# Kernel optimization log

Measured on AMD Instinct MI355X. Metric: run time of the kernel, lower is better.

The kernel has to match this reference:

```python
import jax, jax.numpy as jnp
import numpy as np

# dims: T=max seq len, B=batch, D=d_embed, H=d_hidden, NR=n_roles, NH=n_heads
T, B, D, H = 512, 64, 512, 1024
NR, NH = 64, 8
HD = H // NH  # per-head hidden


def _lengths():
    # monotonically non-increasing lengths -> valid PackedSequence batch_sizes
    return np.round(np.linspace(T, T // 4, B)).astype(np.int32)


def _packed_idx(lengths):
    batch_sizes = np.array([(lengths > t).sum() for t in range(T)], dtype=np.int64)
    # flat row index into padded [T*B] for each packed token (time-major)
    return np.concatenate([t * B + np.arange(batch_sizes[t]) for t in range(T)]).astype(np.int32)


def setup_inputs() -> dict:
    key = jax.random.key(0)
    ks = jax.random.split(key, 12)
    lengths = _lengths()
    idx = _packed_idx(lengths)
    total = int(idx.shape[0])  # 20480
    s = lambda k, shape, sc=1.0: (jax.random.normal(k, shape, jnp.float32) * sc)
    return {
        'x': s(ks[0], (total, D)),
        'idx': jnp.asarray(idx),
        'lengths': jnp.asarray(lengths),
        'basis0': s(ks[1], (NR, H)),  # frozen role basis (requires_grad=False)
        'basis1': s(ks[2], (NR, H)),
        'Wx0': s(ks[3], (2 * H, D), 0.02), 'bx0': jnp.zeros((2 * H,), jnp.float32),
        'Wh0': s(ks[4], (2 * H, H), 0.02), 'bh0': jnp.zeros((2 * H,), jnp.float32),
        'Wv0': s(ks[5], (2 * H, H), 0.02), 'bv0': jnp.zeros((2 * H,), jnp.float32),
        'Wx1': s(ks[6], (2 * H, H), 0.02), 'bx1': jnp.zeros((2 * H,), jnp.float32),
        'Wh1': s(ks[7], (2 * H, H), 0.02), 'bh1': jnp.zeros((2 * H,), jnp.float32),
        'Wv1': s(ks[8], (2 * H, H), 0.02), 'bv1': jnp.zeros((2 * H,), jnp.float32),
    }


def _tpru_layer(x2fg_pad, Wh, bh, r, u, lengths):
    """Run the sequential TPRU recurrence over padded [T,B,2H] precomputed x2fg.

    Replaces the packed per-timestep Python loop (output[p:q] slicing with
    varying batch sizes) with a full-batch lax.scan; rows of padded timesteps
    beyond a sequence's length are computed but never read into output or hn,
    so the math on valid positions is identical.
    """
    h0 = jnp.zeros((B, H), x2fg_pad.dtype)
    hn0 = jnp.zeros((B, H), x2fg_pad.dtype)

    def step(carry, inp):
        h, hn = carry
        x2fg_t, t = inp
        fg = h @ Wh.T + bh + x2fg_t                 # [B, 2H]
        f, g = jnp.split(fg, 2, axis=-1)
        fh = f.reshape(B, NH, HD)
        # unbind: attention over roles per head
        scores = jnp.einsum('bnd,rnd->brn', fh, r)   # [B, NR, NH]
        attn = jax.nn.softmax(scores, axis=1)
        # bind: weighted sum of unbinding vectors
        bind = jnp.einsum('brn,rnd->bnd', attn, u).reshape(B, H)
        gate = jax.nn.sigmoid(g)
        h_new = gate * jnp.tanh(bind) + (1.0 - gate) * h
        # hn captures hidden at each sequence's final valid step
        hn = jnp.where((lengths == t + 1)[:, None], h_new, hn)
        return (h_new, hn), h_new

    (_, hn), hs = jax.lax.scan(step, (h0, hn0), (x2fg_pad, jnp.arange(T)))
    return hs, hn  # hs: [T, B, H]


def reference(x, idx, lengths, basis0, basis1, Wx0, bx0, Wh0, bh0, Wv0, bv0,
              Wx1, bx1, Wh1, bh1, Wv1, bv1):
    # unpack packed data [total, D] into padded [T, B, D]
    x_pad = jnp.zeros((T * B, D), x.dtype).at[idx].set(x).reshape(T, B, D)
    # layer 0
    x2fg = x_pad @ Wx0.T + bx0                       # [T, B, 2H]
    v = (basis0 @ Wv0.T + bv0).reshape(NR, NH, 2 * HD)
    hs, hn0 = _tpru_layer(x2fg, Wh0, bh0, v[..., :HD], v[..., HD:], lengths)
    # layer 1 (input dim is now H)
    x2fg = hs @ Wx1.T + bx1
    v = (basis1 @ Wv1.T + bv1).reshape(NR, NH, 2 * HD)
    hs, hn1 = _tpru_layer(x2fg, Wh1, bh1, v[..., :HD], v[..., HD:], lengths)
    # repack output (time-major packed order, matching PackedSequence.data)
    packed = hs.reshape(T * B, H)[idx]               # [total, H]
    hn = jnp.stack([hn0, hn1])                       # [n_layers, B, H]
    return packed, hn
```

## Files before the change

kernel.cpp:

```cpp
#include <hip/hip_runtime.h>

typedef _Float16 f16;
typedef _Float16 f16x2 __attribute__((ext_vector_type(2)));
typedef _Float16 f16x4 __attribute__((ext_vector_type(4)));
typedef _Float16 f16x8 __attribute__((ext_vector_type(8)));
typedef float    f32x4 __attribute__((ext_vector_type(4)));

#define TT   512
#define BB   64
#define DD   512
#define HH   1024
#define H2   2048
#define NR_  64
#define NH_  8
#define HD_  128
#define MROWS (TT*BB)
#define RWG  64

#define ALOAD32(p)   __hip_atomic_load((p),  __ATOMIC_RELAXED, __HIP_MEMORY_SCOPE_AGENT)
#define ALOAD64(p)   __hip_atomic_load((p),  __ATOMIC_RELAXED, __HIP_MEMORY_SCOPE_AGENT)
#define ASTORE(p,v)  __hip_atomic_store((p), (v), __ATOMIC_RELAXED, __HIP_MEMORY_SCOPE_AGENT)

__global__ void k_cvt(const float* __restrict__ s, f16* __restrict__ d, int n) {
  int i = blockIdx.x * blockDim.x + threadIdx.x;
  int st = gridDim.x * blockDim.x;
  for (; i < n; i += st) d[i] = (f16)s[i];
}

__global__ void k_scatter(const float* __restrict__ x, const int* __restrict__ idx,
                          f16* __restrict__ xpad, int total) {
  int i = blockIdx.x * blockDim.x + threadIdx.x;
  int st = gridDim.x * blockDim.x;
  int n = total * DD;
  for (; i < n; i += st) {
    int p = i >> 9;
    int j = i & (DD - 1);
    xpad[(size_t)idx[p] * DD + j] = (f16)x[i];
  }
}

__global__ void k_inv(const int* __restrict__ idx, int* __restrict__ inv, int total) {
  int i = blockIdx.x * blockDim.x + threadIdx.x;
  if (i < total) inv[idx[i]] = i;
}

__global__ __launch_bounds__(256)
void k_gemm(const f16* __restrict__ A, const f16* __restrict__ Bw,
            const float* __restrict__ bias, f16* __restrict__ C,
            int N, int K, int Mvalid) {
  __shared__ __align__(16) f16 As[128 * 32];
  __shared__ __align__(16) f16 Bs[128 * 32];
  const int tid  = threadIdx.x;
  const int lane = tid & 63;
  const int wave = tid >> 6;
  const int m0 = blockIdx.y * 128;
  const int n0 = blockIdx.x * 128;
  const int mw = (wave >> 1) * 64;
  const int nw = (wave & 1) * 64;
  const int NT = K >> 5;
  const int c0 = tid * 2;

  float4 pa[2], pb[2];
  auto fetch = [&](int kt) {
#pragma unroll
    for (int i = 0; i < 2; ++i) {
      int c = c0 + i;
      int row = c >> 2, kc = c & 3;
      pa[i] = *(const float4*)&A [(size_t)(m0 + row) * K + kt * 32 + kc * 8];
      pb[i] = *(const float4*)&Bw[(size_t)(n0 + row) * K + kt * 32 + kc * 8];
    }
  };

  f32x4 acc[4][4] = {};
  fetch(0);
  for (int kt = 0; kt < NT; ++kt) {
    __syncthreads();
#pragma unroll
    for (int i = 0; i < 2; ++i) {
      int c = c0 + i;
      *(float4*)&As[c * 8] = pa[i];
      *(float4*)&Bs[c * 8] = pb[i];
    }
    __syncthreads();
    if (kt + 1 < NT) fetch(kt + 1);
    f16x8 af[4], bf[4];
#pragma unroll
    for (int i = 0; i < 4; ++i) {
      af[i] = *(const f16x8*)&As[(mw + i * 16 + (lane & 15)) * 32 + (lane >> 4) * 8];
      bf[i] = *(const f16x8*)&Bs[(nw + i * 16 + (lane & 15)) * 32 + (lane >> 4) * 8];
    }
#pragma unroll
    for (int i = 0; i < 4; ++i)
#pragma unroll
      for (int j = 0; j < 4; ++j)
        acc[i][j] = __builtin_amdgcn_mfma_f32_16x16x32_f16(af[i], bf[j], acc[i][j], 0, 0, 0);
  }

#pragma unroll
  for (int j = 0; j < 4; ++j) {
    int col = n0 + nw + j * 16 + (lane & 15);
    float bv = bias[col];
#pragma unroll
    for (int i = 0; i < 4; ++i) {
#pragma unroll
      for (int r = 0; r < 4; ++r) {
        int row = m0 + mw + i * 16 + (lane >> 4) * 4 + r;
        if (row < Mvalid) C[(size_t)row * N + col] = (f16)(acc[i][j][r] + bv);
      }
    }
  }
}

__device__ __forceinline__ void gbar(int* flags, int epoch) {
  __syncthreads();
  const int tid = threadIdx.x;
  if (tid == 0) ASTORE(&flags[blockIdx.x], epoch);
  if (tid < RWG) {
    while (ALOAD32(&flags[tid]) < epoch) __builtin_amdgcn_s_sleep(1);
  }
  __syncthreads();
}

__global__ __launch_bounds__(512, 2)
void k_rec(const f16* __restrict__ Wh16, const float* __restrict__ bh,
           const f16* __restrict__ v16,  const f16* __restrict__ x2fg,
           f16* __restrict__ hfrag, float* __restrict__ fgbuf,
           f16* __restrict__ hs_out, float* __restrict__ out_packed,
           float* __restrict__ hn_out,
           const int* __restrict__ inv, const int* __restrict__ lgt,
           int* __restrict__ flags, int epoch0)
{
  __shared__ __align__(16) f16   Wlds[32 * 2 * 64 * 8];
  __shared__ __align__(16) f16x4 Rq[32 * 64];
  __shared__ __align__(16) f16x4 Uq[16 * 2 * 64];
  __shared__ __align__(16) f32x4 pbuf[8][64];
  __shared__ __align__(16) float fbuf[8][128];
  __shared__ __align__(16) float abuf[8][64];

  const int tid  = threadIdx.x;
  const int lane = tid & 63;
  const int wave = tid >> 6;
  const int wg   = blockIdx.x;
  const int cs   = wg;
  const int rt   = wave & 3;
  const int kh   = wave >> 2;
  const int nh   = wg >> 3;
  const int b    = ((wg & 7) << 3) + wave;
  const int cf   = nh * HD_;

  for (int i = tid; i < 32 * 2 * 64; i += 512) {
    int kk = i >> 7;
    int nt = (i >> 6) & 1;
    int ln = i & 63;
    int col = cs * 32 + nt * 16 + (ln & 15);
    int kg  = kk * 32 + (ln >> 4) * 8;
    *(float4*)&Wlds[(size_t)i * 8] = *(const float4*)&Wh16[(size_t)col * HH + kg];
  }
  for (int e = tid; e < 32 * 64; e += 512) {
    int i = e >> 6, role = e & 63;
    Rq[e] = *(const f16x4*)&v16[(size_t)role * H2 + nh * 256 + 4 * i];
  }
  for (int e = tid; e < 16 * 2 * 64; e += 512) {
    int i = e >> 7, half = (e >> 6) & 1, l = e & 63;
    int r0 = 4 * i + 2 * half;
    const f16* u0 = &v16[(size_t)r0 * H2 + nh * 256 + 128 + 2 * l];
    const f16* u1 = &v16[(size_t)(r0 + 1) * H2 + nh * 256 + 128 + 2 * l];
    f16x4 tv; tv.x = u0[0]; tv.y = u0[1]; tv.z = u1[0]; tv.w = u1[1];
    Uq[e] = tv;
  }
  __syncthreads();

  const int d0 = cf + 2 * lane;
  const float2 bf2 = *(const float2*)&bh[d0];
  const float2 bg2 = *(const float2*)&bh[HH + d0];
  const int lb = lgt[b];
  float ho0 = 0.f, ho1 = 0.f;
  int ep = epoch0;
  const char* hb0 = (const char*)hfrag + (((size_t)kh * 64 + rt) * 64 + lane) * 16;
  const char* fp  = (const char*)fgbuf + (((size_t)b * H2) + d0) * 4;
  const char* gp  = fp + (size_t)HH * 4;

  for (int t = 0; t < TT; ++t) {
    const size_t row = (size_t)t * BB + b;
    const f16* xr = x2fg + row * H2;
    f16x2 xf = *(const f16x2*)&xr[d0];
    f16x2 xg = *(const f16x2*)&xr[HH + d0];
    int   p  = inv[row];

    f32x4 acc0 = {0.f, 0.f, 0.f, 0.f}, acc1 = acc0;
    {
      float4 hb[16];
#pragma unroll
      for (int j = 0; j < 16; ++j) {
        asm volatile("global_load_dwordx4 %0, %1, off sc0 sc1"
                     : "=v"(hb[j]) : "v"(hb0 + (size_t)j * 4096));
      }
      asm volatile("s_waitcnt vmcnt(0)" ::: "memory");
      __builtin_amdgcn_sched_barrier(0);
#pragma unroll
      for (int j = 0; j < 16; ++j) {
        int kk = kh * 16 + j;
        f16x8 af = __builtin_bit_cast(f16x8, hb[j]);
        f16x8 b0 = *(const f16x8*)&Wlds[((kk * 2 + 0) * 64 + lane) * 8];
        f16x8 b1 = *(const f16x8*)&Wlds[((kk * 2 + 1) * 64 + lane) * 8];
        acc0 = __builtin_amdgcn_mfma_f32_16x16x32_f16(af, b0, acc0, 0, 0, 0);
        acc1 = __builtin_amdgcn_mfma_f32_16x16x32_f16(af, b1, acc1, 0, 0, 0);
      }
    }
    pbuf[wave][lane] = (kh == 0) ? acc1 : acc0;
    __syncthreads();
    {
      f32x4 acc = ((kh == 0) ? acc0 : acc1) + pbuf[wave ^ 4][lane];
      const int col = cs * 32 + kh * 16 + (lane & 15);
      const int r0  = rt * 16 + (lane >> 4) * 4;
#pragma unroll
      for (int r = 0; r < 4; ++r) ASTORE(&fgbuf[(size_t)(r0 + r) * H2 + col], acc[r]);
    }
    gbar(flags, ++ep);

    float2 fv, gv;
    asm volatile("global_load_dwordx2 %0, %1, off sc0 sc1" : "=v"(fv) : "v"(fp));
    asm volatile("global_load_dwordx2 %0, %1, off sc0 sc1" : "=v"(gv) : "v"(gp));
    asm volatile("s_waitcnt vmcnt(0)" ::: "memory");
    __builtin_amdgcn_sched_barrier(0);
    float f0 = fv.x + bf2.x + (float)xf.x;
    float f1 = fv.y + bf2.y + (float)xf.y;
    float g0 = gv.x + bg2.x + (float)xg.x;
    float g1 = gv.y + bg2.y + (float)xg.y;
    *(float2*)&fbuf[wave][2 * lane] = make_float2(f0, f1);
    float s = 0.f;
#pragma unroll
    for (int i = 0; i < 32; ++i) {
      float4 fvv = *(const float4*)&fbuf[wave][4 * i];
      f16x4 rv = Rq[i * 64 + lane];
      s = fmaf(fvv.x, (float)rv.x, s);
      s = fmaf(fvv.y, (float)rv.y, s);
      s = fmaf(fvv.z, (float)rv.z, s);
      s = fmaf(fvv.w, (float)rv.w, s);
    }
    float mx = s;
#pragma unroll
    for (int off = 32; off > 0; off >>= 1) mx = fmaxf(mx, __shfl_xor(mx, off));
    float e = expf(s - mx);
    float sum = e;
#pragma unroll
    for (int off = 32; off > 0; off >>= 1) sum += __shfl_xor(sum, off);
    abuf[wave][lane] = e / sum;
    float bd0 = 0.f, bd1 = 0.f;
#pragma unroll
    for (int i = 0; i < 16; ++i) {
      float4 av = *(const float4*)&abuf[wave][4 * i];
      f16x4 u01 = Uq[(i * 2 + 0) * 64 + lane];
      f16x4 u23 = Uq[(i * 2 + 1) * 64 + lane];
      bd0 = fmaf(av.x, (float)u01.x, bd0); bd1 = fmaf(av.x, (float)u01.y, bd1);
      bd0 = fmaf(av.y, (float)u01.z, bd0); bd1 = fmaf(av.y, (float)u01.w, bd1);
      bd0 = fmaf(av.z, (float)u23.x, bd0); bd1 = fmaf(av.z, (float)u23.y, bd1);
      bd0 = fmaf(av.w, (float)u23.z, bd0); bd1 = fmaf(av.w, (float)u23.w, bd1);
    }
    float gt0 = 1.f / (1.f + expf(-g0));
    float gt1 = 1.f / (1.f + expf(-g1));
    float hv0 = gt0 * tanhf(bd0) + (1.f - gt0) * ho0;
    float hv1 = gt1 * tanhf(bd1) + (1.f - gt1) * ho1;
    ho0 = hv0; ho1 = hv1;
    {
      const int k0 = d0;
      unsigned hp = (unsigned)__builtin_bit_cast(unsigned short, (f16)hv0)
                  | ((unsigned)__builtin_bit_cast(unsigned short, (f16)hv1) << 16);
      size_t ui = (((size_t)(k0 >> 5) * 4 + (b >> 4)) * 64
                   + ((b & 15) + (((k0 >> 3) & 3) << 4))) * 4 + ((k0 & 7) >> 1);
      ASTORE((unsigned*)hfrag + ui, hp);
    }
    gbar(flags, ++ep);

    if (hs_out) {
      f16x2 hp2; hp2.x = (f16)ho0; hp2.y = (f16)ho1;
      *(f16x2*)&hs_out[row * HH + d0] = hp2;
    }
    if (out_packed && p >= 0) {
      *(float2*)&out_packed[(size_t)p * HH + d0] = make_float2(ho0, ho1);
    }
    if (lb == t + 1) {
      *(float2*)&hn_out[(size_t)b * HH + d0] = make_float2(ho0, ho1);
    }
  }
}

extern "C" void kernel_launch(void* const* d_in, const int* in_sizes, int n_in,
                              void* d_out, int out_size, void* d_ws, size_t ws_size,
                              hipStream_t stream) {
  const float* x      = (const float*)d_in[0];
  const int*   idx    = (const int*)d_in[1];
  const int*   lgt    = (const int*)d_in[2];
  const float* basis0 = (const float*)d_in[3];
  const float* basis1 = (const float*)d_in[4];
  const float* Wx0 = (const float*)d_in[5];  const float* bx0 = (const float*)d_in[6];
  const float* Wh0 = (const float*)d_in[7];  const float* bh0 = (const float*)d_in[8];
  const float* Wv0 = (const float*)d_in[9];  const float* bv0 = (const float*)d_in[10];
  const float* Wx1 = (const float*)d_in[11]; const float* bx1 = (const float*)d_in[12];
  const float* Wh1 = (const float*)d_in[13]; const float* bh1 = (const float*)d_in[14];
  const float* Wv1 = (const float*)d_in[15]; const float* bv1 = (const float*)d_in[16];
  const int total = in_sizes[1];

  char* ws = (char*)d_ws;
  size_t off = 0;
  auto alloc = [&](size_t bytes) -> void* {
    void* p = (void*)(ws + off);
    off += (bytes + 255) & ~(size_t)255;
    return p;
  };

  int*   flags   = (int*)alloc(RWG * 4);
  int*   inv     = (int*)alloc((size_t)MROWS * 4);
  f16*   xpad    = (f16*)alloc((size_t)MROWS * DD * 2);
  f16*   x2fg    = (f16*)alloc((size_t)MROWS * H2 * 2);
  f16*   hfrag   = (f16*)alloc((size_t)BB * HH * 2);
  float* fgbuf   = (float*)alloc((size_t)BB * H2 * 4);
  f16* Wx0h = (f16*)alloc((size_t)H2 * DD * 2);
  f16* Wh0h = (f16*)alloc((size_t)H2 * HH * 2);
  f16* Wv0h = (f16*)alloc((size_t)H2 * HH * 2);
  f16* Wx1h = (f16*)alloc((size_t)H2 * HH * 2);
  f16* Wh1h = (f16*)alloc((size_t)H2 * HH * 2);
  f16* Wv1h = (f16*)alloc((size_t)H2 * HH * 2);
  f16* bas0h = (f16*)alloc((size_t)128 * HH * 2);
  f16* bas1h = (f16*)alloc((size_t)128 * HH * 2);
  f16* v0h = (f16*)alloc((size_t)NR_ * H2 * 2);
  f16* v1h = (f16*)alloc((size_t)NR_ * H2 * 2);

  float* out = (float*)d_out;
  float* hn0 = out + (size_t)total * HH;
  float* hn1 = hn0 + (size_t)BB * HH;
  f16* hs0 = (f16*)d_out;

  (void)hipMemsetAsync(flags, 0, RWG * 4, stream);
  (void)hipMemsetAsync(inv, 0xFF, (size_t)MROWS * 4, stream);
  (void)hipMemsetAsync(xpad, 0, (size_t)MROWS * DD * 2, stream);
  (void)hipMemsetAsync(bas0h, 0, (size_t)128 * HH * 2, stream);
  (void)hipMemsetAsync(bas1h, 0, (size_t)128 * HH * 2, stream);
  (void)hipMemsetAsync(hfrag, 0, (size_t)BB * HH * 2, stream);

  k_cvt<<<512, 256, 0, stream>>>(Wx0, Wx0h, H2 * DD);
  k_cvt<<<512, 256, 0, stream>>>(Wh0, Wh0h, H2 * HH);
  k_cvt<<<512, 256, 0, stream>>>(Wv0, Wv0h, H2 * HH);
  k_cvt<<<512, 256, 0, stream>>>(Wx1, Wx1h, H2 * HH);
  k_cvt<<<512, 256, 0, stream>>>(Wh1, Wh1h, H2 * HH);
  k_cvt<<<512, 256, 0, stream>>>(Wv1, Wv1h, H2 * HH);
  k_cvt<<<64, 256, 0, stream>>>(basis0, bas0h, NR_ * HH);
  k_cvt<<<64, 256, 0, stream>>>(basis1, bas1h, NR_ * HH);
  k_scatter<<<2048, 256, 0, stream>>>(x, idx, xpad, total);
  k_inv<<<(total + 255) / 256, 256, 0, stream>>>(idx, inv, total);

  dim3 gv(16, 1);
  k_gemm<<<gv, 256, 0, stream>>>(bas0h, Wv0h, bv0, v0h, H2, HH, NR_);
  k_gemm<<<gv, 256, 0, stream>>>(bas1h, Wv1h, bv1, v1h, H2, HH, NR_);

  dim3 gx(H2 / 128, MROWS / 128);
  k_gemm<<<gx, 256, 0, stream>>>(xpad, Wx0h, bx0, x2fg, H2, DD, MROWS);

  k_rec<<<RWG, 512, 0, stream>>>(Wh0h, bh0, v0h, x2fg, hfrag, fgbuf,
                                 hs0, nullptr, hn0, inv, lgt, flags, 0);

  (void)hipMemsetAsync(hfrag, 0, (size_t)BB * HH * 2, stream);

  k_gemm<<<gx, 256, 0, stream>>>(hs0, Wx1h, bx1, x2fg, H2, HH, MROWS);

  k_rec<<<RWG, 512, 0, stream>>>(Wh1h, bh1, v1h, x2fg, hfrag, fgbuf,
                                 nullptr, out, hn1, inv, lgt, flags, 2 * TT);
}
```

Before: 11.52 ms.

## Split recurrent GEMM K across workgroup pairs with dual partial fg buffers

```diff
diff --git a/kernel.cpp b/kernel.cpp
--- a/kernel.cpp
+++ b/kernel.cpp
@@ -18,7 +18,6 @@
 #define RWG  64
 
 #define ALOAD32(p)   __hip_atomic_load((p),  __ATOMIC_RELAXED, __HIP_MEMORY_SCOPE_AGENT)
-#define ALOAD64(p)   __hip_atomic_load((p),  __ATOMIC_RELAXED, __HIP_MEMORY_SCOPE_AGENT)
 #define ASTORE(p,v)  __hip_atomic_store((p), (v), __ATOMIC_RELAXED, __HIP_MEMORY_SCOPE_AGENT)
 
 __global__ void k_cvt(const float* __restrict__ s, f16* __restrict__ d, int n) {
@@ -130,10 +129,10 @@
            const int* __restrict__ inv, const int* __restrict__ lgt,
            int* __restrict__ flags, int epoch0)
 {
-  __shared__ __align__(16) f16   Wlds[32 * 2 * 64 * 8];
+  __shared__ __align__(16) f16   Wlds[16 * 4 * 64 * 8];
   __shared__ __align__(16) f16x4 Rq[32 * 64];
   __shared__ __align__(16) f16x4 Uq[16 * 2 * 64];
-  __shared__ __align__(16) f32x4 pbuf[8][64];
+  __shared__ __align__(16) f32x4 pbuf[8][2][64];
   __shared__ __align__(16) float fbuf[8][128];
   __shared__ __align__(16) float abuf[8][64];
 
@@ -141,19 +140,20 @@
   const int lane = tid & 63;
   const int wave = tid >> 6;
   const int wg   = blockIdx.x;
-  const int cs   = wg;
+  const int cs   = wg >> 1;
+  const int kh   = wg & 1;
   const int rt   = wave & 3;
-  const int kh   = wave >> 2;
+  const int kq   = wave >> 2;
   const int nh   = wg >> 3;
   const int b    = ((wg & 7) << 3) + wave;
   const int cf   = nh * HD_;
 
-  for (int i = tid; i < 32 * 2 * 64; i += 512) {
-    int kk = i >> 7;
-    int nt = (i >> 6) & 1;
+  for (int i = tid; i < 16 * 4 * 64; i += 512) {
+    int kk = i >> 8;
+    int nt = (i >> 6) & 3;
     int ln = i & 63;
-    int col = cs * 32 + nt * 16 + (ln & 15);
-    int kg  = kk * 32 + (ln >> 4) * 8;
+    int col = cs * 64 + nt * 16 + (ln & 15);
+    int kg  = kh * 512 + kk * 32 + (ln >> 4) * 8;
     *(float4*)&Wlds[(size_t)i * 8] = *(const float4*)&Wh16[(size_t)col * HH + kg];
   }
   for (int e = tid; e < 32 * 64; e += 512) {
@@ -176,9 +176,10 @@
   const int lb = lgt[b];
   float ho0 = 0.f, ho1 = 0.f;
   int ep = epoch0;
-  const char* hb0 = (const char*)hfrag + (((size_t)kh * 64 + rt) * 64 + lane) * 16;
-  const char* fp  = (const char*)fgbuf + (((size_t)b * H2) + d0) * 4;
-  const char* gp  = fp + (size_t)HH * 4;
+  const char* hb0 = (const char*)hfrag
+                  + ((((size_t)kh * 16 + kq * 8) * 4 + rt) * 64 + lane) * 16;
+  const char* fp0 = (const char*)fgbuf + (((size_t)b * H2) + d0) * 4;
+  const char* fp1 = fp0 + (size_t)BB * H2 * 4;
 
   for (int t = 0; t < TT; ++t) {
     const size_t row = (size_t)t * BB + b;
@@ -187,46 +188,59 @@
     f16x2 xg = *(const f16x2*)&xr[HH + d0];
     int   p  = inv[row];
 
-    f32x4 acc0 = {0.f, 0.f, 0.f, 0.f}, acc1 = acc0;
+    f32x4 acc[4] = {};
     {
-      float4 hb[16];
-#pragma unroll
-      for (int j = 0; j < 16; ++j) {
+      float4 hb[8];
+#pragma unroll
+      for (int j = 0; j < 8; ++j) {
         asm volatile("global_load_dwordx4 %0, %1, off sc0 sc1"
                      : "=v"(hb[j]) : "v"(hb0 + (size_t)j * 4096));
       }
       asm volatile("s_waitcnt vmcnt(0)" ::: "memory");
       __builtin_amdgcn_sched_barrier(0);
 #pragma unroll
-      for (int j = 0; j < 16; ++j) {
-        int kk = kh * 16 + j;
+      for (int j = 0; j < 8; ++j) {
+        int kk = kq * 8 + j;
         f16x8 af = __builtin_bit_cast(f16x8, hb[j]);
-        f16x8 b0 = *(const f16x8*)&Wlds[((kk * 2 + 0) * 64 + lane) * 8];
-        f16x8 b1 = *(const f16x8*)&Wlds[((kk * 2 + 1) * 64 + lane) * 8];
-        acc0 = __builtin_amdgcn_mfma_f32_16x16x32_f16(af, b0, acc0, 0, 0, 0);
-        acc1 = __builtin_amdgcn_mfma_f32_16x16x32_f16(af, b1, acc1, 0, 0, 0);
+#pragma unroll
+        for (int ct = 0; ct < 4; ++ct) {
+          f16x8 bf = *(const f16x8*)&Wlds[((kk * 4 + ct) * 64 + lane) * 8];
+          acc[ct] = __builtin_amdgcn_mfma_f32_16x16x32_f16(af, bf, acc[ct], 0, 0, 0);
+        }
       }
     }
-    pbuf[wave][lane] = (kh == 0) ? acc1 : acc0;
+    {
+      const int oq = kq ^ 1;
+      pbuf[wave][0][lane] = acc[2 * oq];
+      pbuf[wave][1][lane] = acc[2 * oq + 1];
+    }
     __syncthreads();
     {
-      f32x4 acc = ((kh == 0) ? acc0 : acc1) + pbuf[wave ^ 4][lane];
-      const int col = cs * 32 + kh * 16 + (lane & 15);
-      const int r0  = rt * 16 + (lane >> 4) * 4;
-#pragma unroll
-      for (int r = 0; r < 4; ++r) ASTORE(&fgbuf[(size_t)(r0 + r) * H2 + col], acc[r]);
+      const int pw = wave ^ 4;
+      f32x4 a0 = acc[2 * kq]     + pbuf[pw][0][lane];
+      f32x4 a1 = acc[2 * kq + 1] + pbuf[pw][1][lane];
+      float* fgp = fgbuf + (size_t)kh * BB * H2;
+      const int col0 = cs * 64 + (2 * kq) * 16 + (lane & 15);
+      const int r0   = rt * 16 + (lane >> 4) * 4;
+#pragma unroll
+      for (int r = 0; r < 4; ++r) {
+        ASTORE(&fgp[(size_t)(r0 + r) * H2 + col0],      a0[r]);
+        ASTORE(&fgp[(size_t)(r0 + r) * H2 + col0 + 16], a1[r]);
+      }
     }
     gbar(flags, ++ep);
 
-    float2 fv, gv;
-    asm volatile("global_load_dwordx2 %0, %1, off sc0 sc1" : "=v"(fv) : "v"(fp));
-    asm volatile("global_load_dwordx2 %0, %1, off sc0 sc1" : "=v"(gv) : "v"(gp));
+    float2 fva, fvb, gva, gvb;
+    asm volatile("global_load_dwordx2 %0, %1, off sc0 sc1" : "=v"(fva) : "v"(fp0));
+    asm volatile("global_load_dwordx2 %0, %1, off sc0 sc1" : "=v"(fvb) : "v"(fp1));
+    asm volatile("global_load_dwordx2 %0, %1, off sc0 sc1" : "=v"(gva) : "v"(fp0 + (size_t)HH * 4));
+    asm volatile("global_load_dwordx2 %0, %1, off sc0 sc1" : "=v"(gvb) : "v"(fp1 + (size_t)HH * 4));
     asm volatile("s_waitcnt vmcnt(0)" ::: "memory");
     __builtin_amdgcn_sched_barrier(0);
-    float f0 = fv.x + bf2.x + (float)xf.x;
-    float f1 = fv.y + bf2.y + (float)xf.y;
-    float g0 = gv.x + bg2.x + (float)xg.x;
-    float g1 = gv.y + bg2.y + (float)xg.y;
+    float f0 = fva.x + fvb.x + bf2.x + (float)xf.x;
+    float f1 = fva.y + fvb.y + bf2.y + (float)xf.y;
+    float g0 = gva.x + gvb.x + bg2.x + (float)xg.x;
+    float g1 = gva.y + gvb.y + bg2.y + (float)xg.y;
     *(float2*)&fbuf[wave][2 * lane] = make_float2(f0, f1);
     float s = 0.f;
 #pragma unroll
@@ -314,7 +328,7 @@
   f16*   xpad    = (f16*)alloc((size_t)MROWS * DD * 2);
   f16*   x2fg    = (f16*)alloc((size_t)MROWS * H2 * 2);
   f16*   hfrag   = (f16*)alloc((size_t)BB * HH * 2);
-  float* fgbuf   = (float*)alloc((size_t)BB * H2 * 4);
+  float* fgbuf   = (float*)alloc((size_t)2 * BB * H2 * 4);
   f16* Wx0h = (f16*)alloc((size_t)H2 * DD * 2);
   f16* Wh0h = (f16*)alloc((size_t)H2 * HH * 2);
   f16* Wv0h = (f16*)alloc((size_t)H2 * HH * 2);
```

Measured after the change: 12.77 ms. 10.8% more time.

## Replace global barriers with targeted flag waits and double-buffered hidden state

Applied to the files above, without the earlier changes.

```diff
diff --git a/kernel.cpp b/kernel.cpp
--- a/kernel.cpp
+++ b/kernel.cpp
@@ -18,7 +18,6 @@
 #define RWG  64
 
 #define ALOAD32(p)   __hip_atomic_load((p),  __ATOMIC_RELAXED, __HIP_MEMORY_SCOPE_AGENT)
-#define ALOAD64(p)   __hip_atomic_load((p),  __ATOMIC_RELAXED, __HIP_MEMORY_SCOPE_AGENT)
 #define ASTORE(p,v)  __hip_atomic_store((p), (v), __ATOMIC_RELAXED, __HIP_MEMORY_SCOPE_AGENT)
 
 __global__ void k_cvt(const float* __restrict__ s, f16* __restrict__ d, int n) {
@@ -111,16 +110,6 @@
   }
 }
 
-__device__ __forceinline__ void gbar(int* flags, int epoch) {
-  __syncthreads();
-  const int tid = threadIdx.x;
-  if (tid == 0) ASTORE(&flags[blockIdx.x], epoch);
-  if (tid < RWG) {
-    while (ALOAD32(&flags[tid]) < epoch) __builtin_amdgcn_s_sleep(1);
-  }
-  __syncthreads();
-}
-
 __global__ __launch_bounds__(512, 2)
 void k_rec(const f16* __restrict__ Wh16, const float* __restrict__ bh,
            const f16* __restrict__ v16,  const f16* __restrict__ x2fg,
@@ -128,7 +117,7 @@
            f16* __restrict__ hs_out, float* __restrict__ out_packed,
            float* __restrict__ hn_out,
            const int* __restrict__ inv, const int* __restrict__ lgt,
-           int* __restrict__ flags, int epoch0)
+           int* __restrict__ Afl, int* __restrict__ Bfl, int epoch0)
 {
   __shared__ __align__(16) f16   Wlds[32 * 2 * 64 * 8];
   __shared__ __align__(16) f16x4 Rq[32 * 64];
@@ -175,20 +164,33 @@
   const float2 bg2 = *(const float2*)&bh[HH + d0];
   const int lb = lgt[b];
   float ho0 = 0.f, ho1 = 0.f;
-  int ep = epoch0;
-  const char* hb0 = (const char*)hfrag + (((size_t)kh * 64 + rt) * 64 + lane) * 16;
+  const int pidx = (lane < 4) ? (4 * nh + lane)
+                 : (lane < 8) ? (28 + 4 * nh + lane)
+                 : wg;
+  const size_t hoff = (((size_t)kh * 64 + rt) * 64 + lane) * 16;
+  const char* hbase0 = (const char*)hfrag;
+  const char* hbase1 = (const char*)hfrag + (size_t)BB * HH * 2;
+  unsigned* hw32 = (unsigned*)hfrag;
   const char* fp  = (const char*)fgbuf + (((size_t)b * H2) + d0) * 4;
   const char* gp  = fp + (size_t)HH * 4;
 
   for (int t = 0; t < TT; ++t) {
+    const int e = epoch0 + t + 1;
     const size_t row = (size_t)t * BB + b;
     const f16* xr = x2fg + row * H2;
     f16x2 xf = *(const f16x2*)&xr[d0];
     f16x2 xg = *(const f16x2*)&xr[HH + d0];
     int   p  = inv[row];
 
+    for (;;) {
+      int v = ALOAD32(&Bfl[lane]);
+      if (__all(v >= e - 1)) break;
+      __builtin_amdgcn_s_sleep(1);
+    }
+
     f32x4 acc0 = {0.f, 0.f, 0.f, 0.f}, acc1 = acc0;
     {
+      const char* hb0 = ((t & 1) ? hbase0 : hbase1) + hoff;
       float4 hb[16];
 #pragma unroll
       for (int j = 0; j < 16; ++j) {
@@ -216,7 +218,14 @@
 #pragma unroll
       for (int r = 0; r < 4; ++r) ASTORE(&fgbuf[(size_t)(r0 + r) * H2 + col], acc[r]);
     }
-    gbar(flags, ++ep);
+    __syncthreads();
+    if (tid == 0) ASTORE(&Afl[wg], e);
+
+    for (;;) {
+      int v = ALOAD32(&Afl[pidx]);
+      if (__all((lane >= 8) | (v >= e))) break;
+      __builtin_amdgcn_s_sleep(1);
+    }
 
     float2 fv, gv;
     asm volatile("global_load_dwordx2 %0, %1, off sc0 sc1" : "=v"(fv) : "v"(fp));
@@ -241,11 +250,11 @@
     float mx = s;
 #pragma unroll
     for (int off = 32; off > 0; off >>= 1) mx = fmaxf(mx, __shfl_xor(mx, off));
-    float e = expf(s - mx);
-    float sum = e;
+    float e2 = expf(s - mx);
+    float sum = e2;
 #pragma unroll
     for (int off = 32; off > 0; off >>= 1) sum += __shfl_xor(sum, off);
-    abuf[wave][lane] = e / sum;
+    abuf[wave][lane] = e2 / sum;
     float bd0 = 0.f, bd1 = 0.f;
 #pragma unroll
     for (int i = 0; i < 16; ++i) {
@@ -268,9 +277,10 @@
                   | ((unsigned)__builtin_bit_cast(unsigned short, (f16)hv1) << 16);
       size_t ui = (((size_t)(k0 >> 5) * 4 + (b >> 4)) * 64
                    + ((b & 15) + (((k0 >> 3) & 3) << 4))) * 4 + ((k0 & 7) >> 1);
-      ASTORE((unsigned*)hfrag + ui, hp);
-    }
-    gbar(flags, ++ep);
+      ASTORE(hw32 + (size_t)(t & 1) * (BB * HH / 2) + ui, hp);
+    }
+    __syncthreads();
+    if (tid == 0) ASTORE(&Bfl[wg], e);
 
     if (hs_out) {
       f16x2 hp2; hp2.x = (f16)ho0; hp2.y = (f16)ho1;
@@ -309,11 +319,12 @@
     return p;
   };
 
-  int*   flags   = (int*)alloc(RWG * 4);
+  int*   Afl     = (int*)alloc(RWG * 4);
+  int*   Bfl     = (int*)alloc(RWG * 4);
   int*   inv     = (int*)alloc((size_t)MROWS * 4);
   f16*   xpad    = (f16*)alloc((size_t)MROWS * DD * 2);
   f16*   x2fg    = (f16*)alloc((size_t)MROWS * H2 * 2);
-  f16*   hfrag   = (f16*)alloc((size_t)BB * HH * 2);
+  f16*   hfrag   = (f16*)alloc((size_t)2 * BB * HH * 2);
   float* fgbuf   = (float*)alloc((size_t)BB * H2 * 4);
   f16* Wx0h = (f16*)alloc((size_t)H2 * DD * 2);
   f16* Wh0h = (f16*)alloc((size_t)H2 * HH * 2);
@@ -331,12 +342,13 @@
   float* hn1 = hn0 + (size_t)BB * HH;
   f16* hs0 = (f16*)d_out;
 
-  (void)hipMemsetAsync(flags, 0, RWG * 4, stream);
+  (void)hipMemsetAsync(Afl, 0, RWG * 4, stream);
+  (void)hipMemsetAsync(Bfl, 0, RWG * 4, stream);
   (void)hipMemsetAsync(inv, 0xFF, (size_t)MROWS * 4, stream);
   (void)hipMemsetAsync(xpad, 0, (size_t)MROWS * DD * 2, stream);
   (void)hipMemsetAsync(bas0h, 0, (size_t)128 * HH * 2, stream);
   (void)hipMemsetAsync(bas1h, 0, (size_t)128 * HH * 2, stream);
-  (void)hipMemsetAsync(hfrag, 0, (size_t)BB * HH * 2, stream);
+  (void)hipMemsetAsync(hfrag, 0, (size_t)2 * BB * HH * 2, stream);
 
   k_cvt<<<512, 256, 0, stream>>>(Wx0, Wx0h, H2 * DD);
   k_cvt<<<512, 256, 0, stream>>>(Wh0, Wh0h, H2 * HH);
@@ -357,12 +369,12 @@
   k_gemm<<<gx, 256, 0, stream>>>(xpad, Wx0h, bx0, x2fg, H2, DD, MROWS);
 
   k_rec<<<RWG, 512, 0, stream>>>(Wh0h, bh0, v0h, x2fg, hfrag, fgbuf,
-                                 hs0, nullptr, hn0, inv, lgt, flags, 0);
-
-  (void)hipMemsetAsync(hfrag, 0, (size_t)BB * HH * 2, stream);
+                                 hs0, nullptr, hn0, inv, lgt, Afl, Bfl, 0);
+
+  (void)hipMemsetAsync(hfrag, 0, (size_t)2 * BB * HH * 2, stream);
 
   k_gemm<<<gx, 256, 0, stream>>>(hs0, Wx1h, bx1, x2fg, H2, HH, MROWS);
 
   k_rec<<<RWG, 512, 0, stream>>>(Wh1h, bh1, v1h, x2fg, hfrag, fgbuf,
-                                 nullptr, out, hn1, inv, lgt, flags, 2 * TT);
-}
+                                 nullptr, out, hn1, inv, lgt, Afl, Bfl, TT);
+}
```

New measurement: 9.800 ms. 1.18x faster.
